# Performance work log

Measured on AMD Instinct MI355X. Metric: run time of the kernel, lower is better.

## Reference

```python
import jax, jax.numpy as jnp
import numpy as np

N_NODES = 100000
N_EDGES = 1600000
F = 64
UNITS = 64


def setup_inputs() -> dict:
    key = jax.random.key(0)
    k = jax.random.split(key, 8)
    x = jax.random.normal(k[0], (N_NODES, F), dtype=jnp.float32)
    edge_index = jax.random.randint(k[1], (2, N_EDGES), 0, N_NODES, dtype=jnp.int32)
    edge_weight = jnp.ones((N_EDGES,), dtype=jnp.float32)
    # glorot-uniform-ish params
    def glorot(kk, shape):
        lim = np.sqrt(6.0 / (shape[0] + shape[1]))
        return jax.random.uniform(kk, shape, dtype=jnp.float32, minval=-lim, maxval=lim)
    mlp_kernel = glorot(k[2], (F, UNITS))
    mlp_bias = jnp.zeros((UNITS,), dtype=jnp.float32)
    neighs_kernel = glorot(k[3], (UNITS, UNITS))
    self_kernel = glorot(k[4], (F, UNITS))
    bias = jnp.zeros((2 * UNITS,), dtype=jnp.float32)
    return {"x": x, "edge_index": edge_index, "edge_weight": edge_weight,
            "mlp_kernel": mlp_kernel, "mlp_bias": mlp_bias,
            "neighs_kernel": neighs_kernel, "self_kernel": self_kernel, "bias": bias}


def reference(x, edge_index, edge_weight, mlp_kernel, mlp_bias, neighs_kernel, self_kernel, bias):
    num_nodes = x.shape[0]
    row, col = edge_index[0], edge_index[1]
    # gcn_mapper: neighbor message scaled by edge weight (original forces weights to 1)
    neighbor_x = x[col] * edge_weight[:, None]            # [E, F]
    h = jax.nn.relu(neighbor_x @ mlp_kernel + mlp_bias)   # [E, U]
    # unsorted_segment_mean over destination row (empty segments -> 0, matching TF)
    seg_sum = jax.ops.segment_sum(h, row, num_segments=num_nodes)              # [N, U]
    cnt = jax.ops.segment_sum(jnp.ones_like(row, dtype=h.dtype), row, num_segments=num_nodes)
    reduced_h = seg_sum / jnp.maximum(cnt, 1.0)[:, None]
    from_neighs = reduced_h @ neighs_kernel               # [N, U]
    from_x = x @ self_kernel                              # [N, U]
    out = jnp.concatenate([from_neighs, from_x], axis=1) + bias
    out = jax.nn.relu(out)                                # [N, 2U]
    return out
```

## Files before the change

kernel.cpp:

```cpp
#include <hip/hip_runtime.h>

#define MAXSLICE 12544
#define NBH 32

static __device__ __forceinline__ float relu_f(float v) { return fmaxf(v, 0.f); }

static __device__ __forceinline__ unsigned short f2bf(float f) {
  unsigned u = __float_as_uint(f);
  u += 0x7fffu + ((u >> 16) & 1u);
  return (unsigned short)(u >> 16);
}
static __device__ __forceinline__ float bf2f(unsigned short h) {
  return __uint_as_float(((unsigned)h) << 16);
}

__global__ __launch_bounds__(256) void k_node_dual_gemm(
    const float* __restrict__ x, const float* __restrict__ mk,
    const float* __restrict__ sk, const float* __restrict__ bias,
    unsigned short* __restrict__ xwh, float* __restrict__ out, int n_nodes)
{
  __shared__ float s_mk[64][64];
  __shared__ float s_sk[64][64];
  __shared__ float s_xT[64][68];
  const int tid = threadIdx.x;
  for (int i = tid; i < 4096; i += 256) {
    s_mk[i >> 6][i & 63] = mk[i];
    s_sk[i >> 6][i & 63] = sk[i];
  }
  const int node0 = blockIdx.x * 64;
  for (int i = tid; i < 4096; i += 256) {
    int nl = i >> 6, f = i & 63;
    int n = node0 + nl;
    s_xT[f][nl] = (n < n_nodes) ? x[(size_t)n * 64 + f] : 0.f;
  }
  __syncthreads();
  const int g  = tid >> 4;
  const int ub = (tid & 15) * 4;
  float am[4][4] = {{0.f}};
  float as[4][4] = {{0.f}};
  for (int f = 0; f < 64; ++f) {
    float4 wm = *(const float4*)&s_mk[f][ub];
    float4 ws = *(const float4*)&s_sk[f][ub];
    float4 xv = *(const float4*)&s_xT[f][4 * g];
    const float xs[4] = {xv.x, xv.y, xv.z, xv.w};
#pragma unroll
    for (int j = 0; j < 4; ++j) {
      am[j][0] += xs[j] * wm.x; am[j][1] += xs[j] * wm.y;
      am[j][2] += xs[j] * wm.z; am[j][3] += xs[j] * wm.w;
      as[j][0] += xs[j] * ws.x; as[j][1] += xs[j] * ws.y;
      as[j][2] += xs[j] * ws.z; as[j][3] += xs[j] * ws.w;
    }
  }
  float4 bv = *(const float4*)&bias[64 + ub];
#pragma unroll
  for (int j = 0; j < 4; ++j) {
    int n = node0 + 4 * g + j;
    if (n >= n_nodes) break;
    ushort4 o1 = make_ushort4(f2bf(am[j][0]), f2bf(am[j][1]),
                              f2bf(am[j][2]), f2bf(am[j][3]));
    *(ushort4*)&xwh[(size_t)n * 64 + ub] = o1;
    *(float4*)&out[(size_t)n * 128 + 64 + ub] =
        make_float4(relu_f(as[j][0] + bv.x), relu_f(as[j][1] + bv.y),
                    relu_f(as[j][2] + bv.z), relu_f(as[j][3] + bv.w));
  }
}

__global__ __launch_bounds__(256) void k_count(
    const int* __restrict__ row, int* __restrict__ cnt, int n_edges)
{
  int e = blockIdx.x * 256 + threadIdx.x;
  if (e < n_edges) atomicAdd(&cnt[row[e]], 1);
}

__global__ __launch_bounds__(256) void k_build_sliced(
    const int* __restrict__ row, const int* __restrict__ col,
    const float* __restrict__ ew, int* __restrict__ off,
    int2* __restrict__ elist, int n_edges, int n_nodes)
{
  const int slice = blockIdx.x & 7;
  const int vb    = blockIdx.x >> 3;
  const int nvb   = gridDim.x >> 3;
  const int sliceN = (n_nodes + 7) >> 3;
  const int lo = slice * sliceN;
  const int hi = min(lo + sliceN, n_nodes);
  for (int e = vb * 256 + threadIdx.x; e < n_edges; e += nvb * 256) {
    int r = row[e];
    if (r >= lo && r < hi) {
      int pos = atomicAdd(&off[r], 1);
      elist[pos] = make_int2(col[e], __float_as_int(ew[e]));
    }
  }
}

__global__ __launch_bounds__(1024) void k_bsum(
    const int* __restrict__ cnt, int* __restrict__ bsum, int n)
{
  __shared__ int s[1024];
  int tid = threadIdx.x;
  int i = blockIdx.x * 1024 + tid;
  s[tid] = (i < n) ? cnt[i] : 0;
  __syncthreads();
  for (int d = 512; d > 0; d >>= 1) {
    if (tid < d) s[tid] += s[tid + d];
    __syncthreads();
  }
  if (tid == 0) bsum[blockIdx.x] = s[0];
}

__global__ __launch_bounds__(1024) void k_boffs(
    const int* __restrict__ cnt, const int* __restrict__ bsum,
    int* __restrict__ off, int n, int nb)
{
  __shared__ int s[1024];
  __shared__ int sp[128];
  int tid = threadIdx.x;
  if (tid < 128) {
    int acc = 0;
    for (int j = tid; j < blockIdx.x && j < nb; j += 128) acc += bsum[j];
    sp[tid] = acc;
  }
  int i = blockIdx.x * 1024 + tid;
  int v = (i < n) ? cnt[i] : 0;
  s[tid] = v;
  __syncthreads();
  for (int d = 64; d > 0; d >>= 1) {
    if (tid < d) sp[tid] += sp[tid + d];
    __syncthreads();
  }
  for (int d = 1; d < 1024; d <<= 1) {
    int t = (tid >= d) ? s[tid - d] : 0;
    __syncthreads();
    s[tid] += t;
    __syncthreads();
  }
  if (i < n) off[i] = s[tid] - v + sp[0];
}

__global__ __launch_bounds__(256) void k_bin(
    const int* __restrict__ row, const int* __restrict__ col,
    const float* __restrict__ ew,
    int* __restrict__ brow, int2* __restrict__ bpair,
    int* __restrict__ bcur, int n_edges, int sliceN, int cap)
{
  __shared__ int  s_wcnt[4][8];
  __shared__ int  s_tot[8];
  __shared__ int  s_toff[8];
  __shared__ int  s_gaddr[8];
  __shared__ int  s_rowst[1024];
  __shared__ int2 s_pairst[1024];
  const int tid  = threadIdx.x;
  const int wave = tid >> 6;
  const int lane = tid & 63;
  const unsigned usliceN = (unsigned)sliceN;
  const int stride = gridDim.x * 1024;
  for (int e0 = blockIdx.x * 1024; e0 < n_edges; e0 += stride) {
    const int e = e0 + 4 * tid;
    int   rr[4], cc[4];
    float ww[4];
    int   ss[4];
    if (e + 3 < n_edges) {
      int4 r4   = *(const int4*)&row[e];
      int4 c4   = *(const int4*)&col[e];
      float4 w4 = *(const float4*)&ew[e];
      rr[0] = r4.x; rr[1] = r4.y; rr[2] = r4.z; rr[3] = r4.w;
      cc[0] = c4.x; cc[1] = c4.y; cc[2] = c4.z; cc[3] = c4.w;
      ww[0] = w4.x; ww[1] = w4.y; ww[2] = w4.z; ww[3] = w4.w;
#pragma unroll
      for (int j = 0; j < 4; ++j) ss[j] = (int)((unsigned)rr[j] / usliceN);
    } else {
#pragma unroll
      for (int j = 0; j < 4; ++j) {
        int ej = e + j;
        bool v = ej < n_edges;
        rr[j] = v ? row[ej] : 0;
        cc[j] = v ? col[ej] : 0;
        ww[j] = v ? ew[ej]  : 0.f;
        ss[j] = v ? (int)((unsigned)rr[j] / usliceN) : -1;
      }
    }
#pragma unroll
    for (int b = 0; b < 8; ++b) {
      int c = 0;
#pragma unroll
      for (int j = 0; j < 4; ++j) c += __popcll(__ballot(ss[j] == b));
      if (lane == 0) s_wcnt[wave][b] = c;
    }
    __syncthreads();
    if (wave == 0 && lane < 8) {
      const int b = lane;
      int t0 = s_wcnt[0][b], t1 = s_wcnt[1][b], t2 = s_wcnt[2][b], t3 = s_wcnt[3][b];
      int tot = t0 + t1 + t2 + t3;
      s_tot[b] = tot;
      s_wcnt[0][b] = 0;
      s_wcnt[1][b] = t0;
      s_wcnt[2][b] = t0 + t1;
      s_wcnt[3][b] = t0 + t1 + t2;
      int gbase = tot ? atomicAdd(&bcur[b], tot) : 0;
      int pre = 0;
#pragma unroll
      for (int j2 = 0; j2 < 8; ++j2) pre += (j2 < b) ? s_tot[j2] : 0;
      s_toff[b]  = pre;
      s_gaddr[b] = b * cap + gbase - pre;
    }
    __syncthreads();
#pragma unroll
    for (int b = 0; b < 8; ++b) {
      const int sb = s_toff[b] + s_wcnt[wave][b];
      int off_local = 0;
#pragma unroll
      for (int j = 0; j < 4; ++j) {
        unsigned long long mm = __ballot(ss[j] == b);
        if (ss[j] == b) {
          int rank = __popcll(mm & ((1ull << lane) - 1ull));
          int slot = sb + off_local + rank;
          s_rowst[slot]  = rr[j];
          s_pairst[slot] = make_int2(cc[j], __float_as_int(ww[j]));
        }
        off_local += __popcll(mm);
      }
    }
    __syncthreads();
    const int total = s_toff[7] + s_tot[7];
    for (int i2 = tid; i2 < total; i2 += 256) {
      int b = 0;
#pragma unroll
      for (int j2 = 1; j2 < 8; ++j2) b += (i2 >= s_toff[j2]) ? 1 : 0;
      int a = s_gaddr[b] + i2;
      if (a < (b + 1) * cap) {
        brow[a]  = s_rowst[i2];
        bpair[a] = s_pairst[i2];
      }
    }
    __syncthreads();
  }
}

__global__ __launch_bounds__(256) void k_hist(
    const int* __restrict__ brow, const int* __restrict__ bcur,
    int* __restrict__ hist, int cap, int chunk, int sliceN)
{
  __shared__ int h[MAXSLICE];
  const int s   = blockIdx.x & 7;
  const int blk = blockIdx.x >> 3;
  const int tid = threadIdx.x;
  for (int i = tid; i < MAXSLICE; i += 256) h[i] = 0;
  __syncthreads();
  const int n_s  = min(bcur[s], cap);
  const int lo_e = blk * chunk;
  const int hi_e = min(lo_e + chunk, n_s);
  const int base = s * cap;
  const int lo   = s * sliceN;
  for (int i = lo_e + tid; i < hi_e; i += 256) {
    atomicAdd(&h[brow[base + i] - lo], 1);
  }
  __syncthreads();
  int* hrow = hist + (size_t)(s * NBH + blk) * MAXSLICE;
  for (int i = tid; i < MAXSLICE / 4; i += 256) {
    ((int4*)hrow)[i] = ((const int4*)h)[i];
  }
}

__global__ __launch_bounds__(256) void k_colscan(
    int* __restrict__ hist, int* __restrict__ cnt, int sliceN, int n_nodes)
{
  const int s  = blockIdx.x & 7;
  const int cb = blockIdx.x >> 3;
  const int b0 = cb * 1024 + threadIdx.x * 4;
  if (b0 >= sliceN) return;
  int4 acc = make_int4(0, 0, 0, 0);
  int* hs = hist + (size_t)s * NBH * MAXSLICE;
#pragma unroll 4
  for (int blk = 0; blk < NBH; ++blk) {
    int4* p = (int4*)(hs + (size_t)blk * MAXSLICE + b0);
    int4 v = *p;
    *p = acc;
    acc.x += v.x; acc.y += v.y; acc.z += v.z; acc.w += v.w;
  }
  const int node = s * sliceN + b0;
  if (b0 + 3 < sliceN && node + 3 < n_nodes) {
    *(int4*)&cnt[node] = acc;
  } else {
    int a[4] = {acc.x, acc.y, acc.z, acc.w};
    for (int j = 0; j < 4; ++j)
      if (b0 + j < sliceN && node + j < n_nodes) cnt[node + j] = a[j];
  }
}

__global__ __launch_bounds__(256) void k_place(
    const int* __restrict__ brow, const int2* __restrict__ bpair,
    const int* __restrict__ bcur, const int* __restrict__ hist,
    const int* __restrict__ off, int2* __restrict__ elist,
    int cap, int chunk, int sliceN, int n_nodes)
{
  __shared__ int cur[MAXSLICE];
  const int s   = blockIdx.x & 7;
  const int blk = blockIdx.x >> 3;
  const int tid = threadIdx.x;
  const int lo  = s * sliceN;
  const int hi  = min(lo + sliceN, n_nodes);
  const int nb  = hi - lo;
  const int* hrow = hist + (size_t)(s * NBH + blk) * MAXSLICE;
  for (int i = tid; i < nb; i += 256) cur[i] = off[lo + i] + hrow[i];
  __syncthreads();
  const int n_s  = min(bcur[s], cap);
  const int lo_e = blk * chunk;
  const int hi_e = min(lo_e + chunk, n_s);
  const int base = s * cap;
  for (int i = lo_e + tid; i < hi_e; i += 256) {
    int r = brow[base + i] - lo;
    int p = atomicAdd(&cur[r], 1);
    elist[p] = bpair[base + i];
  }
}

__global__ __launch_bounds__(256) void k_scatter(
    const int* __restrict__ brow, const int2* __restrict__ bpair,
    const int* __restrict__ bcur, int* __restrict__ off,
    int2* __restrict__ elist, int cap)
{
  const int s   = blockIdx.x & 7;
  const int vb  = blockIdx.x >> 3;
  const int nvb = gridDim.x >> 3;
  const int n   = min(bcur[s], cap);
  const int base = s * cap;
  for (int i = vb * 256 + threadIdx.x; i < n; i += nvb * 256) {
    int r = brow[base + i];
    int pos = atomicAdd(&off[r], 1);
    elist[pos] = bpair[base + i];
  }
}

__global__ __launch_bounds__(256) void k_fused_reduce_gemm(
    const int* __restrict__ cnt, const int* __restrict__ off,
    const int2* __restrict__ elist, const unsigned short* __restrict__ xwh,
    const float* __restrict__ mb, const float* __restrict__ nk,
    const float* __restrict__ bias, float* __restrict__ out, int n_nodes,
    int starts)
{
  __shared__ float s_nk[64][64];
  __shared__ float s_rh[16][68];
  const int tid = threadIdx.x;
  for (int i = tid; i < 1024; i += 256) {
    *(float4*)&s_nk[0][4 * i] = *(const float4*)&nk[4 * i];
  }
  const int node_l = tid >> 4;
  const int q = tid & 15;
  const int n = blockIdx.x * 16 + node_l;
  float4 acc = make_float4(0.f, 0.f, 0.f, 0.f);
  if (n < n_nodes) {
    const float4 mbq = *(const float4*)&mb[4 * q];
    const int c = cnt[n];
    int i = off[n] - (starts ? 0 : c);
    const int end = i + c;
    for (; i + 8 <= end; i += 8) {
      int2 e[8];
#pragma unroll
      for (int j = 0; j < 8; ++j) e[j] = elist[i + j];
      ushort4 u[8];
#pragma unroll
      for (int j = 0; j < 8; ++j)
        u[j] = *(const ushort4*)&xwh[(size_t)e[j].x * 64 + 4 * q];
#pragma unroll
      for (int j = 0; j < 8; ++j) {
        float w = __int_as_float(e[j].y);
        acc.x += relu_f(w * bf2f(u[j].x) + mbq.x);
        acc.y += relu_f(w * bf2f(u[j].y) + mbq.y);
        acc.z += relu_f(w * bf2f(u[j].z) + mbq.z);
        acc.w += relu_f(w * bf2f(u[j].w) + mbq.w);
      }
    }
    if (i + 4 <= end) {
      int2 e[4];
#pragma unroll
      for (int j = 0; j < 4; ++j) e[j] = elist[i + j];
      ushort4 u[4];
#pragma unroll
      for (int j = 0; j < 4; ++j)
        u[j] = *(const ushort4*)&xwh[(size_t)e[j].x * 64 + 4 * q];
#pragma unroll
      for (int j = 0; j < 4; ++j) {
        float w = __int_as_float(e[j].y);
        acc.x += relu_f(w * bf2f(u[j].x) + mbq.x);
        acc.y += relu_f(w * bf2f(u[j].y) + mbq.y);
        acc.z += relu_f(w * bf2f(u[j].z) + mbq.z);
        acc.w += relu_f(w * bf2f(u[j].w) + mbq.w);
      }
      i += 4;
    }
    for (; i < end; ++i) {
      int2 e0 = elist[i];
      ushort4 u0 = *(const ushort4*)&xwh[(size_t)e0.x * 64 + 4 * q];
      float w0 = __int_as_float(e0.y);
      acc.x += relu_f(w0 * bf2f(u0.x) + mbq.x);
      acc.y += relu_f(w0 * bf2f(u0.y) + mbq.y);
      acc.z += relu_f(w0 * bf2f(u0.z) + mbq.z);
      acc.w += relu_f(w0 * bf2f(u0.w) + mbq.w);
    }
    const float inv = 1.0f / fmaxf((float)c, 1.0f);
    acc.x *= inv; acc.y *= inv; acc.z *= inv; acc.w *= inv;
  }
  *(float4*)&s_rh[node_l][4 * q] = acc;
  __syncthreads();
  float4 o = make_float4(0.f, 0.f, 0.f, 0.f);
  for (int f = 0; f < 64; ++f) {
    float rv = s_rh[node_l][f];
    float4 wv = *(const float4*)&s_nk[f][4 * q];
    o.x += rv * wv.x; o.y += rv * wv.y; o.z += rv * wv.z; o.w += rv * wv.w;
  }
  if (n < n_nodes) {
    float4 bv = *(const float4*)&bias[4 * q];
    *(float4*)&out[(size_t)n * 128 + 4 * q] =
        make_float4(relu_f(o.x + bv.x), relu_f(o.y + bv.y),
                    relu_f(o.z + bv.z), relu_f(o.w + bv.w));
  }
}

extern "C" void kernel_launch(void* const* d_in, const int* in_sizes, int n_in,
                              void* d_out, int out_size, void* d_ws, size_t ws_size,
                              hipStream_t stream) {
  const float* x    = (const float*)d_in[0];
  const int*   ei   = (const int*)d_in[1];
  const float* ew   = (const float*)d_in[2];
  const float* mk   = (const float*)d_in[3];
  const float* mb   = (const float*)d_in[4];
  const float* nk   = (const float*)d_in[5];
  const float* sk   = (const float*)d_in[6];
  const float* bias = (const float*)d_in[7];
  float* out = (float*)d_out;

  const int n_nodes = in_sizes[0] / 64;
  const int n_edges = in_sizes[2];
  const int* row = ei;
  const int* col = ei + n_edges;

  unsigned short* xwh = (unsigned short*)d_ws;
  int*  cnt  = (int*)(xwh + (size_t)n_nodes * 64);
  int*  bcur = cnt + n_nodes;
  int*  off  = bcur + 8;
  int*  bsum = off + n_nodes;
  size_t ebytes = ((size_t)((char*)(bsum + 128) - (char*)d_ws) + 7) & ~(size_t)7;
  int2* elist = (int2*)((char*)d_ws + ebytes);
  const int cap = (n_edges >> 3) + 8192;
  int*  brow  = (int*)(elist + n_edges);
  size_t pboff = (((size_t)((char*)(brow + (size_t)8 * cap) - (char*)d_ws)) + 7) & ~(size_t)7;
  int2* bpair = (int2*)((char*)d_ws + pboff);
  size_t need_b = (size_t)((char*)(bpair + (size_t)8 * cap) - (char*)d_ws);
  size_t hoff = (need_b + 15) & ~(size_t)15;
  int*  hist  = (int*)((char*)d_ws + hoff);
  size_t need_a = hoff + (size_t)8 * NBH * MAXSLICE * sizeof(int);

  const int nb_scan = (n_nodes + 1023) / 1024;
  const int sliceN = (n_nodes + 7) >> 3;
  const int nbn = (n_nodes + 63) / 64;
  const int nbf = (n_nodes + 15) / 16;
  const int chunk = (cap + NBH - 1) / NBH;

  if (ws_size >= need_a && sliceN <= MAXSLICE) {
    hipMemsetAsync(bcur, 0, 8 * sizeof(int), stream);
    k_node_dual_gemm<<<nbn, 256, 0, stream>>>(x, mk, sk, bias, xwh, out, n_nodes);
    int nbb = (n_edges + 1023) / 1024;
    if (nbb > 2048) nbb = 2048;
    k_bin<<<nbb, 256, 0, stream>>>(row, col, ew, brow, bpair, bcur,
                                   n_edges, sliceN, cap);
    k_hist<<<8 * NBH, 256, 0, stream>>>(brow, bcur, hist, cap, chunk, sliceN);
    const int ncb = (sliceN + 1023) / 1024;
    k_colscan<<<8 * ncb, 256, 0, stream>>>(hist, cnt, sliceN, n_nodes);
    k_bsum<<<nb_scan, 1024, 0, stream>>>(cnt, bsum, n_nodes);
    k_boffs<<<nb_scan, 1024, 0, stream>>>(cnt, bsum, off, n_nodes, nb_scan);
    k_place<<<8 * NBH, 256, 0, stream>>>(brow, bpair, bcur, hist, off,
                                         elist, cap, chunk, sliceN, n_nodes);
    k_fused_reduce_gemm<<<nbf, 256, 0, stream>>>(cnt, off, elist, xwh, mb, nk,
                                                 bias, out, n_nodes, 1);
  } else if (ws_size >= need_b) {
    hipMemsetAsync(cnt, 0, (size_t)(n_nodes + 8) * sizeof(int), stream);
    k_node_dual_gemm<<<nbn, 256, 0, stream>>>(x, mk, sk, bias, xwh, out, n_nodes);
    int nbb = (n_edges + 1023) / 1024;
    if (nbb > 2048) nbb = 2048;
    k_bin<<<nbb, 256, 0, stream>>>(row, col, ew, brow, bpair, bcur,
                                   n_edges, sliceN, cap);
    const int nbe = (n_edges + 255) / 256;
    k_count<<<nbe, 256, 0, stream>>>(row, cnt, n_edges);
    k_bsum<<<nb_scan, 1024, 0, stream>>>(cnt, bsum, n_nodes);
    k_boffs<<<nb_scan, 1024, 0, stream>>>(cnt, bsum, off, n_nodes, nb_scan);
    k_scatter<<<1024, 256, 0, stream>>>(brow, bpair, bcur, off, elist, cap);
    k_fused_reduce_gemm<<<nbf, 256, 0, stream>>>(cnt, off, elist, xwh, mb, nk,
                                                 bias, out, n_nodes, 0);
  } else {
    hipMemsetAsync(cnt, 0, (size_t)n_nodes * sizeof(int), stream);
    k_node_dual_gemm<<<nbn, 256, 0, stream>>>(x, mk, sk, bias, xwh, out, n_nodes);
    const int nbe = (n_edges + 255) / 256;
    k_count<<<nbe, 256, 0, stream>>>(row, cnt, n_edges);
    k_bsum<<<nb_scan, 1024, 0, stream>>>(cnt, bsum, n_nodes);
    k_boffs<<<nb_scan, 1024, 0, stream>>>(cnt, bsum, off, n_nodes, nb_scan);
    k_build_sliced<<<1024, 256, 0, stream>>>(row, col, ew, off, elist,
                                             n_edges, n_nodes);
    k_fused_reduce_gemm<<<nbf, 256, 0, stream>>>(cnt, off, elist, xwh, mb, nk,
                                                 bias, out, n_nodes, 0);
  }
}
```

Before: 256.8 us.

## Balance edge work across thread groups in fused reduce-gemm via edge-range chunking

```diff
diff --git a/kernel.cpp b/kernel.cpp
--- a/kernel.cpp
+++ b/kernel.cpp
@@ -331,76 +331,84 @@
 }
 
 __global__ __launch_bounds__(256) void k_fused_reduce_gemm(
-    const int* __restrict__ cnt, const int* __restrict__ off,
-    const int2* __restrict__ elist, const unsigned short* __restrict__ xwh,
-    const float* __restrict__ mb, const float* __restrict__ nk,
-    const float* __restrict__ bias, float* __restrict__ out, int n_nodes,
-    int starts)
+    const int* __restrict__ off, const int2* __restrict__ elist,
+    const unsigned short* __restrict__ xwh, const float* __restrict__ mb,
+    const float* __restrict__ nk, const float* __restrict__ bias,
+    float* __restrict__ out, int n_nodes, int n_edges, int starts)
 {
   __shared__ float s_nk[64][64];
   __shared__ float s_rh[16][68];
+  __shared__ int   s_off[17];
   const int tid = threadIdx.x;
   for (int i = tid; i < 1024; i += 256) {
     *(float4*)&s_nk[0][4 * i] = *(const float4*)&nk[4 * i];
   }
-  const int node_l = tid >> 4;
+  for (int i = tid; i < 16 * 68; i += 256) ((float*)s_rh)[i] = 0.f;
+  const int n0 = blockIdx.x * 16;
+  if (tid < 17) {
+    int idx = n0 + tid;
+    int b;
+    if (starts) {
+      b = (idx < n_nodes) ? off[idx] : n_edges;
+    } else {
+      b = (idx == 0) ? 0 : ((idx - 1 < n_nodes) ? off[idx - 1] : n_edges);
+    }
+    s_off[tid] = b;
+  }
+  __syncthreads();
+  const int g = tid >> 4;
   const int q = tid & 15;
-  const int n = blockIdx.x * 16 + node_l;
-  float4 acc = make_float4(0.f, 0.f, 0.f, 0.f);
-  if (n < n_nodes) {
-    const float4 mbq = *(const float4*)&mb[4 * q];
-    const int c = cnt[n];
-    int i = off[n] - (starts ? 0 : c);
-    const int end = i + c;
-    for (; i + 8 <= end; i += 8) {
+  const float4 mbq = *(const float4*)&mb[4 * q];
+  const int off0 = s_off[0];
+  const int tot  = s_off[16] - off0;
+  const int chunk = (tot + 15) >> 4;
+  int i = off0 + g * chunk;
+  const int iend = min(i + chunk, off0 + tot);
+  if (i < iend) {
+    int cur = 0;
+    if (s_off[cur + 8] <= i) cur += 8;
+    if (s_off[cur + 4] <= i) cur += 4;
+    if (s_off[cur + 2] <= i) cur += 2;
+    if (s_off[cur + 1] <= i) cur += 1;
+    int hi = s_off[cur + 1];
+    float4 acc = make_float4(0.f, 0.f, 0.f, 0.f);
+    for (;;) {
+      const int k = min(min(hi, iend) - i, 8);
       int2 e[8];
-#pragma unroll
-      for (int j = 0; j < 8; ++j) e[j] = elist[i + j];
       ushort4 u[8];
+#pragma unroll
+      for (int j = 0; j < 8; ++j)
+        e[j] = (j < k) ? elist[i + j] : make_int2(0, 0);
 #pragma unroll
       for (int j = 0; j < 8; ++j)
         u[j] = *(const ushort4*)&xwh[(size_t)e[j].x * 64 + 4 * q];
 #pragma unroll
       for (int j = 0; j < 8; ++j) {
-        float w = __int_as_float(e[j].y);
-        acc.x += relu_f(w * bf2f(u[j].x) + mbq.x);
-        acc.y += relu_f(w * bf2f(u[j].y) + mbq.y);
-        acc.z += relu_f(w * bf2f(u[j].z) + mbq.z);
-        acc.w += relu_f(w * bf2f(u[j].w) + mbq.w);
+        if (j < k) {
+          float w = __int_as_float(e[j].y);
+          acc.x += relu_f(w * bf2f(u[j].x) + mbq.x);
+          acc.y += relu_f(w * bf2f(u[j].y) + mbq.y);
+          acc.z += relu_f(w * bf2f(u[j].z) + mbq.z);
+          acc.w += relu_f(w * bf2f(u[j].w) + mbq.w);
+        }
       }
-    }
-    if (i + 4 <= end) {
-      int2 e[4];
-#pragma unroll
-      for (int j = 0; j < 4; ++j) e[j] = elist[i + j];
-      ushort4 u[4];
-#pragma unroll
-      for (int j = 0; j < 4; ++j)
-        u[j] = *(const ushort4*)&xwh[(size_t)e[j].x * 64 + 4 * q];
-#pragma unroll
-      for (int j = 0; j < 4; ++j) {
-        float w = __int_as_float(e[j].y);
-        acc.x += relu_f(w * bf2f(u[j].x) + mbq.x);
-        acc.y += relu_f(w * bf2f(u[j].y) + mbq.y);
-        acc.z += relu_f(w * bf2f(u[j].z) + mbq.z);
-        acc.w += relu_f(w * bf2f(u[j].w) + mbq.w);
+      i += k;
+      if (i >= hi || i >= iend) {
+        atomicAdd(&s_rh[cur][4 * q + 0], acc.x);
+        atomicAdd(&s_rh[cur][4 * q + 1], acc.y);
+        atomicAdd(&s_rh[cur][4 * q + 2], acc.z);
+        atomicAdd(&s_rh[cur][4 * q + 3], acc.w);
+        if (i >= iend) break;
+        acc = make_float4(0.f, 0.f, 0.f, 0.f);
+        ++cur;
+        while (s_off[cur + 1] <= i) ++cur;
+        hi = s_off[cur + 1];
       }
-      i += 4;
-    }
-    for (; i < end; ++i) {
-      int2 e0 = elist[i];
-      ushort4 u0 = *(const ushort4*)&xwh[(size_t)e0.x * 64 + 4 * q];
-      float w0 = __int_as_float(e0.y);
-      acc.x += relu_f(w0 * bf2f(u0.x) + mbq.x);
-      acc.y += relu_f(w0 * bf2f(u0.y) + mbq.y);
-      acc.z += relu_f(w0 * bf2f(u0.z) + mbq.z);
-      acc.w += relu_f(w0 * bf2f(u0.w) + mbq.w);
-    }
-    const float inv = 1.0f / fmaxf((float)c, 1.0f);
-    acc.x *= inv; acc.y *= inv; acc.z *= inv; acc.w *= inv;
-  }
-  *(float4*)&s_rh[node_l][4 * q] = acc;
-  __syncthreads();
+    }
+  }
+  __syncthreads();
+  const int node_l = g;
+  const int n = n0 + node_l;
   float4 o = make_float4(0.f, 0.f, 0.f, 0.f);
   for (int f = 0; f < 64; ++f) {
     float rv = s_rh[node_l][f];
@@ -408,10 +416,12 @@
     o.x += rv * wv.x; o.y += rv * wv.y; o.z += rv * wv.z; o.w += rv * wv.w;
   }
   if (n < n_nodes) {
+    const int c = s_off[node_l + 1] - s_off[node_l];
+    const float inv = 1.0f / fmaxf((float)c, 1.0f);
     float4 bv = *(const float4*)&bias[4 * q];
     *(float4*)&out[(size_t)n * 128 + 4 * q] =
-        make_float4(relu_f(o.x + bv.x), relu_f(o.y + bv.y),
-                    relu_f(o.z + bv.z), relu_f(o.w + bv.w));
+        make_float4(relu_f(o.x * inv + bv.x), relu_f(o.y * inv + bv.y),
+                    relu_f(o.z * inv + bv.z), relu_f(o.w * inv + bv.w));
   }
 }
 
@@ -469,8 +479,8 @@
     k_boffs<<<nb_scan, 1024, 0, stream>>>(cnt, bsum, off, n_nodes, nb_scan);
     k_place<<<8 * NBH, 256, 0, stream>>>(brow, bpair, bcur, hist, off,
                                          elist, cap, chunk, sliceN, n_nodes);
-    k_fused_reduce_gemm<<<nbf, 256, 0, stream>>>(cnt, off, elist, xwh, mb, nk,
-                                                 bias, out, n_nodes, 1);
+    k_fused_reduce_gemm<<<nbf, 256, 0, stream>>>(off, elist, xwh, mb, nk,
+                                                 bias, out, n_nodes, n_edges, 1);
   } else if (ws_size >= need_b) {
     hipMemsetAsync(cnt, 0, (size_t)(n_nodes + 8) * sizeof(int), stream);
     k_node_dual_gemm<<<nbn, 256, 0, stream>>>(x, mk, sk, bias, xwh, out, n_nodes);
@@ -483,8 +493,8 @@
     k_bsum<<<nb_scan, 1024, 0, stream>>>(cnt, bsum, n_nodes);
     k_boffs<<<nb_scan, 1024, 0, stream>>>(cnt, bsum, off, n_nodes, nb_scan);
     k_scatter<<<1024, 256, 0, stream>>>(brow, bpair, bcur, off, elist, cap);
-    k_fused_reduce_gemm<<<nbf, 256, 0, stream>>>(cnt, off, elist, xwh, mb, nk,
-                                                 bias, out, n_nodes, 0);
+    k_fused_reduce_gemm<<<nbf, 256, 0, stream>>>(off, elist, xwh, mb, nk,
+                                                 bias, out, n_nodes, n_edges, 0);
   } else {
     hipMemsetAsync(cnt, 0, (size_t)n_nodes * sizeof(int), stream);
     k_node_dual_gemm<<<nbn, 256, 0, stream>>>(x, mk, sk, bias, xwh, out, n_nodes);
@@ -494,7 +504,7 @@
     k_boffs<<<nb_scan, 1024, 0, stream>>>(cnt, bsum, off, n_nodes, nb_scan);
     k_build_sliced<<<1024, 256, 0, stream>>>(row, col, ew, off, elist,
                                              n_edges, n_nodes);
-    k_fused_reduce_gemm<<<nbf, 256, 0, stream>>>(cnt, off, elist, xwh, mb, nk,
-                                                 bias, out, n_nodes, 0);
-  }
-}
+    k_fused_reduce_gemm<<<nbf, 256, 0, stream>>>(off, elist, xwh, mb, nk,
+                                                 bias, out, n_nodes, n_edges, 0);
+  }
+}
```

After: 311.4 us. +21.3%, slower.

## Bucket edges by 16-node groups and reduce with shared-memory atomics

Applied to the files above, without the earlier changes.

```diff
diff --git a/kernel.cpp b/kernel.cpp
--- a/kernel.cpp
+++ b/kernel.cpp
@@ -1,6 +1,7 @@
 #include <hip/hip_runtime.h>
 
 #define MAXSLICE 12544
+#define MAXSUB   800
 #define NBH 32
 
 static __device__ __forceinline__ float relu_f(float v) { return fmaxf(v, 0.f); }
@@ -313,24 +314,7 @@
   }
 }
 
-__global__ __launch_bounds__(256) void k_scatter(
-    const int* __restrict__ brow, const int2* __restrict__ bpair,
-    const int* __restrict__ bcur, int* __restrict__ off,
-    int2* __restrict__ elist, int cap)
-{
-  const int s   = blockIdx.x & 7;
-  const int vb  = blockIdx.x >> 3;
-  const int nvb = gridDim.x >> 3;
-  const int n   = min(bcur[s], cap);
-  const int base = s * cap;
-  for (int i = vb * 256 + threadIdx.x; i < n; i += nvb * 256) {
-    int r = brow[base + i];
-    int pos = atomicAdd(&off[r], 1);
-    elist[pos] = bpair[base + i];
-  }
-}
-
-__global__ __launch_bounds__(256) void k_fused_reduce_gemm(
+__global__ __launch_bounds__(256) void k_fused_csr(
     const int* __restrict__ cnt, const int* __restrict__ off,
     const int2* __restrict__ elist, const unsigned short* __restrict__ xwh,
     const float* __restrict__ mb, const float* __restrict__ nk,
@@ -412,6 +396,168 @@
     *(float4*)&out[(size_t)n * 128 + 4 * q] =
         make_float4(relu_f(o.x + bv.x), relu_f(o.y + bv.y),
                     relu_f(o.z + bv.z), relu_f(o.w + bv.w));
+  }
+}
+
+
+__global__ __launch_bounds__(256) void k_hist16(
+    const int* __restrict__ brow, const int* __restrict__ bcur,
+    int* __restrict__ hist, int cap, int chunk, int sliceN)
+{
+  __shared__ int h[MAXSUB];
+  const int s   = blockIdx.x & 7;
+  const int blk = blockIdx.x >> 3;
+  const int tid = threadIdx.x;
+  const int nsub = (sliceN + 15) >> 4;
+  for (int i = tid; i < nsub; i += 256) h[i] = 0;
+  __syncthreads();
+  const int n_s  = min(bcur[s], cap);
+  const int lo_e = blk * chunk;
+  const int hi_e = min(lo_e + chunk, n_s);
+  const int base = s * cap;
+  const int lo   = s * sliceN;
+  for (int i = lo_e + tid; i < hi_e; i += 256) {
+    atomicAdd(&h[(brow[base + i] - lo) >> 4], 1);
+  }
+  __syncthreads();
+  int* hrow = hist + (size_t)(s * NBH + blk) * MAXSUB;
+  for (int i = tid; i < nsub; i += 256) hrow[i] = h[i];
+}
+
+__global__ __launch_bounds__(1024) void k_colscan16(
+    int* __restrict__ hist, const int* __restrict__ bcur,
+    int* __restrict__ off_sub, int cap, int sliceN)
+{
+  __shared__ int s_t[1024];
+  const int s = blockIdx.x;
+  const int tid = threadIdx.x;
+  const int nsub = (sliceN + 15) >> 4;
+  int acc = 0;
+  if (tid < nsub) {
+    int* hs = hist + (size_t)s * NBH * MAXSUB;
+    for (int blk = 0; blk < NBH; ++blk) {
+      int* p = hs + (size_t)blk * MAXSUB + tid;
+      int v = *p;
+      *p = acc;
+      acc += v;
+    }
+  }
+  s_t[tid] = (tid < nsub) ? acc : 0;
+  __syncthreads();
+  for (int d = 1; d < 1024; d <<= 1) {
+    int t = (tid >= d) ? s_t[tid - d] : 0;
+    __syncthreads();
+    s_t[tid] += t;
+    __syncthreads();
+  }
+  int base = 0;
+  for (int b = 0; b < s; ++b) base += min(bcur[b], cap);
+  int excl = (tid == 0) ? 0 : s_t[tid - 1];
+  if (tid < nsub) off_sub[s * nsub + tid] = base + excl;
+  if (s == 7 && tid == 1023) off_sub[8 * nsub] = base + s_t[1023];
+}
+
+__global__ __launch_bounds__(256) void k_place16(
+    const int* __restrict__ brow, const int2* __restrict__ bpair,
+    const int* __restrict__ bcur, const int* __restrict__ hist,
+    const int* __restrict__ off_sub, int2* __restrict__ elist,
+    int cap, int chunk, int sliceN)
+{
+  __shared__ int cur[MAXSUB];
+  const int s   = blockIdx.x & 7;
+  const int blk = blockIdx.x >> 3;
+  const int tid = threadIdx.x;
+  const int nsub = (sliceN + 15) >> 4;
+  const int* hrow = hist + (size_t)(s * NBH + blk) * MAXSUB;
+  for (int i = tid; i < nsub; i += 256) cur[i] = off_sub[s * nsub + i] + hrow[i];
+  __syncthreads();
+  const int n_s  = min(bcur[s], cap);
+  const int lo_e = blk * chunk;
+  const int hi_e = min(lo_e + chunk, n_s);
+  const int base = s * cap;
+  const int lo   = s * sliceN;
+  for (int i = lo_e + tid; i < hi_e; i += 256) {
+    int rloc = brow[base + i] - lo;
+    int p = atomicAdd(&cur[rloc >> 4], 1);
+    int2 pr = bpair[base + i];
+    elist[p] = make_int2(pr.x | ((rloc & 15) << 27), pr.y);
+  }
+}
+
+__global__ __launch_bounds__(256) void k_fused16(
+    const int* __restrict__ off_sub, const int2* __restrict__ elist,
+    const unsigned short* __restrict__ xwh, const float* __restrict__ mb,
+    const float* __restrict__ nk, const float* __restrict__ bias,
+    float* __restrict__ out, int n_nodes, int sliceN)
+{
+  __shared__ float s_nk[64][64];
+  __shared__ float s_rh[16][65];
+  __shared__ int   s_cnt[16];
+  const int tid = threadIdx.x;
+  for (int i = tid; i < 1024; i += 256) {
+    *(float4*)&s_nk[0][4 * i] = *(const float4*)&nk[4 * i];
+  }
+  for (int i = tid; i < 16 * 65; i += 256) ((float*)s_rh)[i] = 0.f;
+  if (tid < 16) s_cnt[tid] = 0;
+  const int s   = blockIdx.x & 7;
+  const int sub = blockIdx.x >> 3;
+  const int nsub = (sliceN + 15) >> 4;
+  const int e0 = off_sub[s * nsub + sub];
+  const int e1 = off_sub[s * nsub + sub + 1];
+  __syncthreads();
+  for (int i = e0 + tid; i < e1; i += 256) {
+    atomicAdd(&s_cnt[((unsigned)elist[i].x) >> 27], 1);
+  }
+  const int g = tid >> 4;
+  const int q = tid & 15;
+  const float4 mbq = *(const float4*)&mb[4 * q];
+  const int m = e1 - e0;
+  const int len = (m + 15) >> 4;
+  int i = e0 + g * len;
+  const int iend = min(i + len, e1);
+  for (; i + 8 <= iend; i += 8) {
+    int2 e[8];
+#pragma unroll
+    for (int j = 0; j < 8; ++j) e[j] = elist[i + j];
+    ushort4 u[8];
+#pragma unroll
+    for (int j = 0; j < 8; ++j)
+      u[j] = *(const ushort4*)&xwh[(size_t)(e[j].x & 0x07FFFFFF) * 64 + 4 * q];
+#pragma unroll
+    for (int j = 0; j < 8; ++j) {
+      float w = __int_as_float(e[j].y);
+      int rl = (unsigned)e[j].x >> 27;
+      atomicAdd(&s_rh[rl][4 * q + 0], relu_f(w * bf2f(u[j].x) + mbq.x));
+      atomicAdd(&s_rh[rl][4 * q + 1], relu_f(w * bf2f(u[j].y) + mbq.y));
+      atomicAdd(&s_rh[rl][4 * q + 2], relu_f(w * bf2f(u[j].z) + mbq.z));
+      atomicAdd(&s_rh[rl][4 * q + 3], relu_f(w * bf2f(u[j].w) + mbq.w));
+    }
+  }
+  for (; i < iend; ++i) {
+    int2 ev = elist[i];
+    ushort4 u0 = *(const ushort4*)&xwh[(size_t)(ev.x & 0x07FFFFFF) * 64 + 4 * q];
+    float w = __int_as_float(ev.y);
+    int rl = (unsigned)ev.x >> 27;
+    atomicAdd(&s_rh[rl][4 * q + 0], relu_f(w * bf2f(u0.x) + mbq.x));
+    atomicAdd(&s_rh[rl][4 * q + 1], relu_f(w * bf2f(u0.y) + mbq.y));
+    atomicAdd(&s_rh[rl][4 * q + 2], relu_f(w * bf2f(u0.z) + mbq.z));
+    atomicAdd(&s_rh[rl][4 * q + 3], relu_f(w * bf2f(u0.w) + mbq.w));
+  }
+  __syncthreads();
+  const int node_l = g;
+  const int n = s * sliceN + sub * 16 + node_l;
+  float4 o = make_float4(0.f, 0.f, 0.f, 0.f);
+  for (int f = 0; f < 64; ++f) {
+    float rv = s_rh[node_l][f];
+    float4 wv = *(const float4*)&s_nk[f][4 * q];
+    o.x += rv * wv.x; o.y += rv * wv.y; o.z += rv * wv.z; o.w += rv * wv.w;
+  }
+  if (n < n_nodes && (sub * 16 + node_l) < sliceN) {
+    const float inv = 1.0f / fmaxf((float)s_cnt[node_l], 1.0f);
+    float4 bv = *(const float4*)&bias[4 * q];
+    *(float4*)&out[(size_t)n * 128 + 4 * q] =
+        make_float4(relu_f(o.x * inv + bv.x), relu_f(o.y * inv + bv.y),
+                    relu_f(o.z * inv + bv.z), relu_f(o.w * inv + bv.w));
   }
 }
 
@@ -451,11 +597,30 @@
 
   const int nb_scan = (n_nodes + 1023) / 1024;
   const int sliceN = (n_nodes + 7) >> 3;
+  const int nsub = (sliceN + 15) >> 4;
   const int nbn = (n_nodes + 63) / 64;
   const int nbf = (n_nodes + 15) / 16;
   const int chunk = (cap + NBH - 1) / NBH;
-
-  if (ws_size >= need_a && sliceN <= MAXSLICE) {
+  int* off_sub = cnt;
+
+  const bool fitsA = (ws_size >= need_a) && (sliceN <= MAXSLICE);
+  const bool subOK = fitsA && (nsub <= MAXSUB) && (n_nodes >= 16) &&
+                     (n_nodes < (1 << 27)) && (8 * nsub + 1 <= n_nodes);
+
+  if (subOK) {
+    hipMemsetAsync(bcur, 0, 8 * sizeof(int), stream);
+    k_node_dual_gemm<<<nbn, 256, 0, stream>>>(x, mk, sk, bias, xwh, out, n_nodes);
+    int nbb = (n_edges + 1023) / 1024;
+    if (nbb > 2048) nbb = 2048;
+    k_bin<<<nbb, 256, 0, stream>>>(row, col, ew, brow, bpair, bcur,
+                                   n_edges, sliceN, cap);
+    k_hist16<<<8 * NBH, 256, 0, stream>>>(brow, bcur, hist, cap, chunk, sliceN);
+    k_colscan16<<<8, 1024, 0, stream>>>(hist, bcur, off_sub, cap, sliceN);
+    k_place16<<<8 * NBH, 256, 0, stream>>>(brow, bpair, bcur, hist, off_sub,
+                                           elist, cap, chunk, sliceN);
+    k_fused16<<<8 * nsub, 256, 0, stream>>>(off_sub, elist, xwh, mb, nk, bias,
+                                            out, n_nodes, sliceN);
+  } else if (fitsA) {
     hipMemsetAsync(bcur, 0, 8 * sizeof(int), stream);
     k_node_dual_gemm<<<nbn, 256, 0, stream>>>(x, mk, sk, bias, xwh, out, n_nodes);
     int nbb = (n_edges + 1023) / 1024;
@@ -469,22 +634,8 @@
     k_boffs<<<nb_scan, 1024, 0, stream>>>(cnt, bsum, off, n_nodes, nb_scan);
     k_place<<<8 * NBH, 256, 0, stream>>>(brow, bpair, bcur, hist, off,
                                          elist, cap, chunk, sliceN, n_nodes);
-    k_fused_reduce_gemm<<<nbf, 256, 0, stream>>>(cnt, off, elist, xwh, mb, nk,
-                                                 bias, out, n_nodes, 1);
-  } else if (ws_size >= need_b) {
-    hipMemsetAsync(cnt, 0, (size_t)(n_nodes + 8) * sizeof(int), stream);
-    k_node_dual_gemm<<<nbn, 256, 0, stream>>>(x, mk, sk, bias, xwh, out, n_nodes);
-    int nbb = (n_edges + 1023) / 1024;
-    if (nbb > 2048) nbb = 2048;
-    k_bin<<<nbb, 256, 0, stream>>>(row, col, ew, brow, bpair, bcur,
-                                   n_edges, sliceN, cap);
-    const int nbe = (n_edges + 255) / 256;
-    k_count<<<nbe, 256, 0, stream>>>(row, cnt, n_edges);
-    k_bsum<<<nb_scan, 1024, 0, stream>>>(cnt, bsum, n_nodes);
-    k_boffs<<<nb_scan, 1024, 0, stream>>>(cnt, bsum, off, n_nodes, nb_scan);
-    k_scatter<<<1024, 256, 0, stream>>>(brow, bpair, bcur, off, elist, cap);
-    k_fused_reduce_gemm<<<nbf, 256, 0, stream>>>(cnt, off, elist, xwh, mb, nk,
-                                                 bias, out, n_nodes, 0);
+    k_fused_csr<<<nbf, 256, 0, stream>>>(cnt, off, elist, xwh, mb, nk,
+                                         bias, out, n_nodes, 1);
   } else {
     hipMemsetAsync(cnt, 0, (size_t)n_nodes * sizeof(int), stream);
     k_node_dual_gemm<<<nbn, 256, 0, stream>>>(x, mk, sk, bias, xwh, out, n_nodes);
@@ -494,7 +645,7 @@
     k_boffs<<<nb_scan, 1024, 0, stream>>>(cnt, bsum, off, n_nodes, nb_scan);
     k_build_sliced<<<1024, 256, 0, stream>>>(row, col, ew, off, elist,
                                              n_edges, n_nodes);
-    k_fused_reduce_gemm<<<nbf, 256, 0, stream>>>(cnt, off, elist, xwh, mb, nk,
-                                                 bias, out, n_nodes, 0);
-  }
-}
+    k_fused_csr<<<nbf, 256, 0, stream>>>(cnt, off, elist, xwh, mb, nk,
+                                         bias, out, n_nodes, 0);
+  }
+}
```

Result: slower. 745.7 us (+190.4%).
